# Kernel tuning notes

Hardware: AMD Instinct MI355X
Metric: run time of the kernel (lower is better)

## Reference

```python
import jax, jax.numpy as jnp
import numpy as np


def _relu(x):
    return jnp.maximum(x, 0.0)


def _wn(V, g):
    # torch weight_norm with dim=None: W = g * V / ||V||_F (scalar g)
    return g * V / jnp.linalg.norm(V)


def _wn_rank(V, g):
    # V: [rank, out, in], g: [rank] -> per-rank weight-normed weights
    n = jnp.sqrt(jnp.sum(V * V, axis=(1, 2), keepdims=True))
    return g[:, None, None] * V / n


def setup_inputs() -> dict:
    key = jax.random.key(0)
    ks = jax.random.split(key, 20)
    B, N, D, H, R, HK, G = 16, 64, 512, 512, 8, 64, 2
    f = lambda i, shape, s=1.0: jax.random.normal(ks[i], shape, dtype=jnp.float32) * s
    u = lambda i, shape: jax.random.uniform(ks[i], shape, dtype=jnp.float32)
    return {
        'v': f(0, (B, N, D)), 'q': f(1, (B, N, D)), 'a': f(2, (B, N, D)),
        'V_v': f(3, (H, D), 0.05), 'g_v': u(4, (1,)), 'b_v': f(5, (H,), 0.05),
        'V_q': f(6, (H, D), 0.05), 'g_q': u(7, (1,)), 'b_q': f(8, (H,), 0.05),
        'V_a': f(9, (H, D), 0.05), 'g_a': u(10, (1,)), 'b_a': f(11, (H,), 0.05),
        'Vn_v': f(12, (R, HK, H), 0.05), 'gn_v': u(13, (R,)), 'bn_v': f(14, (R, HK), 0.05),
        'Vn_qa': f(15, (R, HK, H), 0.05), 'gn_qa': u(16, (R,)), 'bn_qa': f(17, (R, HK), 0.05),
        'T_g': f(18, (R, HK, HK, HK, G), 0.02),  # T_g with h_out=1 squeezed
        'gamma': u(19, (H,)), 'beta': jnp.zeros((H,), jnp.float32),
    }


def reference(v, q, a, V_v, g_v, b_v, V_q, g_q, b_q, V_a, g_a, b_a,
              Vn_v, gn_v, bn_v, Vn_qa, gn_qa, bn_qa, T_g, gamma, beta):
    # Tucker projections (FCNet = weight-normed Linear + ReLU; dropout off in eval)
    v_t = _relu(v @ _wn(V_v, g_v).T + b_v)  # [B, Nv, H]
    q_t = _relu(q @ _wn(V_q, g_q).T + b_q)  # [B, Nq, H]
    a_t = _relu(a @ _wn(V_a, g_a).T + b_a)  # [B, Na, H]

    # Per-rank FCNets, vectorized over the rank loop (q_net and a_net share weights)
    Wv = _wn_rank(Vn_v, gn_v)    # [R, HK, H]
    Wqa = _wn_rank(Vn_qa, gn_qa)  # [R, HK, H]
    v_r = _relu(jnp.einsum('bnh,rkh->brnk', v_t, Wv) + bn_v[None, :, None, :])   # [B,R,Nv,HK]
    q_r = _relu(jnp.einsum('bnh,rkh->brnk', q_t, Wqa) + bn_qa[None, :, None, :])  # [B,R,Nq,HK]
    a_r = _relu(jnp.einsum('bnh,rkh->brnk', a_t, Wqa) + bn_qa[None, :, None, :])  # [B,R,Na,HK]

    # ModeProduct summed over rank: f_emb[b,v,q,m,g] = sum_r T_g[r,h,k,l,g] v_r q_r a_r
    t = jnp.einsum('brvh,rhklg->brvklg', v_r, T_g)
    t = jnp.einsum('brvklg,brqk->brvqlg', t, q_r)
    f_emb = jnp.einsum('brvqlg,brml->bvqmg', t, a_r)  # [B, Nv, Nq, Na, G]

    # logits = einsum('bdv,bvqag,bdqi,bdaj->bdijg').sum(-1).squeeze(3).squeeze(2)
    # with i=j=1 this is: logits[b,d] = sum_{v,q,a,g} v_t f_emb q_t a_t
    t2 = jnp.einsum('bvqag,bad->bvqdg', f_emb, a_t)
    t2 = jnp.einsum('bvqdg,bqd->bvdg', t2, q_t)
    logits = jnp.einsum('bvdg,bvd->bd', t2, v_t)  # [B, H]

    # BatchNorm1d (training-mode batch statistics, eps=1e-5)
    mu = jnp.mean(logits, axis=0)
    var = jnp.var(logits, axis=0)
    logits = (logits - mu) / jnp.sqrt(var + 1e-5) * gamma + beta

    # torch returns f_emb.squeeze(4): no-op since glimpse=2
    return f_emb, logits
```

## Files before the change

kernel.cpp:

```cpp
#include <hip/hip_runtime.h>
#include <hip/hip_fp16.h>
#include <math.h>


typedef _Float16 f16x8 __attribute__((ext_vector_type(8)));
typedef float f32x4 __attribute__((ext_vector_type(4)));

__device__ __forceinline__ unsigned short f2h(float x) {
  _Float16 h = (_Float16)x;
  return __builtin_bit_cast(unsigned short, h);
}

__device__ __forceinline__ int fragoff(int row, int kr) {
  return (((row & 15) + (((kr >> 2) & 3) << 4)) << 3) + (kr & 3) + (((kr >> 4) & 1) << 2);
}

#define WS_NRM 0
#define WS_VT  32
#define WS_QT  (WS_VT + 524288)
#define WS_AT  (WS_QT + 524288)
#define WS_LP  (WS_AT + 524288)
#define WS_LR  (WS_LP + 524288)
#define WS_PRT (WS_LR + 8192)
#define WS_H   (WS_PRT + 1280)
#define H_VR2 0
#define H_QR2 524288
#define H_AR2 1048576
#define H_T2  1572864
#define H_AT16 5767168
#define H_IN16 6291456
#define H_WB16 7864320
#define H_WN16 8650752
#define H_RP16 9175040
#define H_U   10747904

__global__ __launch_bounds__(256) void k_norms_part(
    const float* __restrict__ Vv, const float* __restrict__ Vq, const float* __restrict__ Va,
    const float* __restrict__ Vnv, const float* __restrict__ Vnqa, float* __restrict__ prt)
{
  const int bx = blockIdx.x;
  int n, j;
  const float* base;
  if (bx < 192) {
    n = bx >> 6; j = bx & 63;
    base = (n == 0 ? Vv : n == 1 ? Vq : Va) + j * 4096;
  } else {
    int t = bx - 192;
    n = 3 + (t >> 3); j = t & 7;
    base = (n < 11 ? Vnv + (n - 3) * 32768 : Vnqa + (n - 11) * 32768) + j * 4096;
  }
  const float4* p4 = (const float4*)base;
  float s = 0.f;
  #pragma unroll
  for (int i = 0; i < 4; ++i) {
    float4 x = p4[threadIdx.x + i * 256];
    s += x.x * x.x + x.y * x.y + x.z * x.z + x.w * x.w;
  }
  __shared__ float red[256];
  red[threadIdx.x] = s; __syncthreads();
  for (int off = 128; off > 0; off >>= 1) {
    if (threadIdx.x < off) red[threadIdx.x] += red[threadIdx.x + off];
    __syncthreads();
  }
  if (threadIdx.x == 0) prt[n * 64 + j] = red[0];
}

__global__ __launch_bounds__(64) void k_norms_fin(const float* __restrict__ prt, float* __restrict__ wsn)
{
  const int n = blockIdx.x, t = threadIdx.x;
  const int cnt = (n < 3) ? 64 : 8;
  float s = (t < cnt) ? prt[n * 64 + t] : 0.f;
  #pragma unroll
  for (int off = 32; off > 0; off >>= 1) s += __shfl_down(s, off);
  if (t == 0) wsn[n] = sqrtf(s);
}

__global__ __launch_bounds__(256) void k_inconv16(
    const float* __restrict__ v, const float* __restrict__ q, const float* __restrict__ a,
    unsigned short* __restrict__ IN16)
{
  const int z = blockIdx.y;
  const float4* src = (const float4*)((z == 0) ? v : (z == 1) ? q : a);
  #pragma unroll
  for (int i = 0; i < 8; ++i) {
    int f = blockIdx.x * 2048 + threadIdx.x + i * 256;
    int row = f >> 7, d0 = (f & 127) * 4;
    float4 x = src[f];
    ushort4 pk;
    pk.x = f2h(x.x); pk.y = f2h(x.y); pk.z = f2h(x.z); pk.w = f2h(x.w);
    int lanep = (row & 15) + (((d0 >> 2) & 3) << 4);
    int jb = ((d0 >> 4) & 1) << 2;
    size_t off = ((size_t)(z * 64 + (row >> 4)) * 16 + (d0 >> 5)) * 512 + lanep * 8 + jb;
    *(ushort4*)&IN16[off] = pk;
  }
}

__global__ __launch_bounds__(256) void k_wconv16(
    const float* __restrict__ Wv, const float* __restrict__ Wq, const float* __restrict__ Wa,
    const float* __restrict__ gv, const float* __restrict__ gq, const float* __restrict__ ga,
    const float* __restrict__ wsn, unsigned short* __restrict__ WB16)
{
  const int z = blockIdx.y;
  const float4* src = (const float4*)((z == 0) ? Wv : (z == 1) ? Wq : Wa);
  const float scale = ((z == 0) ? gv[0] : (z == 1) ? gq[0] : ga[0]) / wsn[z];
  #pragma unroll
  for (int i = 0; i < 8; ++i) {
    int f = blockIdx.x * 2048 + threadIdx.x + i * 256;
    int n = f >> 7, d0 = (f & 127) * 4;
    float4 x = src[f];
    ushort4 pk;
    pk.x = f2h(x.x * scale); pk.y = f2h(x.y * scale);
    pk.z = f2h(x.z * scale); pk.w = f2h(x.w * scale);
    int lanep = (n & 15) + (((d0 >> 2) & 3) << 4);
    int jb = ((d0 >> 4) & 1) << 2;
    size_t off = ((size_t)(z * 32 + (n >> 4)) * 16 + (d0 >> 5)) * 512 + lanep * 8 + jb;
    *(ushort4*)&WB16[off] = pk;
  }
}

__global__ __launch_bounds__(256) void k_wnconv16(
    const float* __restrict__ Vnv, const float* __restrict__ Vnqa,
    const float* __restrict__ gnv, const float* __restrict__ gnqa,
    const float* __restrict__ wsn, unsigned short* __restrict__ WN16)
{
  const int zr = blockIdx.x >> 2, sub = blockIdx.x & 3;
  const int zq = zr >> 3, r = zr & 7;
  const float4* src = (const float4*)((zq == 0 ? Vnv : Vnqa) + (size_t)r * 32768);
  const float scale = (zq == 0) ? (gnv[r] / wsn[3 + r]) : (gnqa[r] / wsn[11 + r]);
  #pragma unroll
  for (int i = 0; i < 8; ++i) {
    int f = sub * 2048 + threadIdx.x + i * 256;
    int n = f >> 7, d0 = (f & 127) * 4;
    float4 x = src[f];
    ushort4 pk;
    pk.x = f2h(x.x * scale); pk.y = f2h(x.y * scale);
    pk.z = f2h(x.z * scale); pk.w = f2h(x.w * scale);
    int lanep = (n & 15) + (((d0 >> 2) & 3) << 4);
    int jb = ((d0 >> 4) & 1) << 2;
    size_t off = ((size_t)(zr * 4 + (n >> 4)) * 16 + (d0 >> 5)) * 512 + lanep * 8 + jb;
    *(ushort4*)&WN16[off] = pk;
  }
}

__global__ __launch_bounds__(256) void k_repack2b(const float* __restrict__ Tg, unsigned short* __restrict__ T2)
{
  const int r = blockIdx.x >> 4, lB = blockIdx.x & 15;
  __shared__ unsigned short lds[32768];
  const int tid = threadIdx.x;

  #pragma unroll
  for (int i = 0; i < 32; ++i) {
    int f = tid + i * 256;
    int lpair = f & 1, k = (f >> 1) & 63, h = f >> 7;
    int l0 = lB * 4 + lpair * 2;
    const float4 x = *(const float4*)(Tg + ((size_t)((r * 64 + h) * 64 + k) * 64 + l0) * 2);
    const int el = fragoff(k & 15, h & 31);
    const int ks = h >> 5;
    const int ntr0 = (l0 & 3) * 4 + (k >> 4);
    const int ntr1 = ((l0 + 1) & 3) * 4 + (k >> 4);
    lds[((0 * 16 + ntr0) * 2 + ks) * 512 + el] = f2h(x.x);
    lds[((1 * 16 + ntr0) * 2 + ks) * 512 + el] = f2h(x.y);
    lds[((0 * 16 + ntr1) * 2 + ks) * 512 + el] = f2h(x.z);
    lds[((1 * 16 + ntr1) * 2 + ks) * 512 + el] = f2h(x.w);
  }
  __syncthreads();

  #pragma unroll
  for (int g = 0; g < 2; ++g) {
    unsigned short* dst = T2 + ((size_t)(g * 8 + r) * 256 + lB * 16) * 1024;
    const float4* s = (const float4*)&lds[g * 16384];
    float4* d = (float4*)dst;
    #pragma unroll
    for (int i = 0; i < 8; ++i) d[tid + i * 256] = s[tid + i * 256];
  }
}

__global__ __launch_bounds__(256) void k_proj16(
    const unsigned short* __restrict__ IN16, const unsigned short* __restrict__ WB16,
    const float* __restrict__ bv, const float* __restrict__ bq, const float* __restrict__ ba,
    float* __restrict__ ov, float* __restrict__ oq, float* __restrict__ oa,
    unsigned short* __restrict__ RP16, unsigned short* __restrict__ AT16)
{
  const int nB = blockIdx.x, mB = blockIdx.y, z = blockIdx.z;
  const float* bias = (z == 0) ? bv : (z == 1) ? bq : ba;
  float* out = (z == 0) ? ov : (z == 1) ? oq : oa;
  const int tid = threadIdx.x, lane = tid & 63;
  const int w = __builtin_amdgcn_readfirstlane(tid >> 6);

  f32x4 c[4];
  #pragma unroll
  for (int mt = 0; mt < 4; ++mt) c[mt] = (f32x4){0.f, 0.f, 0.f, 0.f};

  #pragma unroll 4
  for (int ks = 0; ks < 16; ++ks) {
    f16x8 af[4], bfr;
    #pragma unroll
    for (int mt = 0; mt < 4; ++mt)
      af[mt] = *(const f16x8*)&IN16[((size_t)(z * 64 + mB * 4 + mt) * 16 + ks) * 512 + lane * 8];
    bfr = *(const f16x8*)&WB16[((size_t)(z * 32 + nB * 4 + w) * 16 + ks) * 512 + lane * 8];
    #pragma unroll
    for (int mt = 0; mt < 4; ++mt)
      c[mt] = __builtin_amdgcn_mfma_f32_16x16x32_f16(af[mt], bfr, c[mt], 0, 0, 0);
  }

  const int col = nB * 64 + w * 16 + (lane & 15);
  const float bb = bias[col];
  #pragma unroll
  for (int mt = 0; mt < 4; ++mt)
    #pragma unroll
    for (int i = 0; i < 4; ++i) {
      const int row = mB * 64 + mt * 16 + 4 * (lane >> 4) + i;
      float val = fmaxf(c[mt][i] + bb, 0.f);
      unsigned short hv = f2h(val);
      out[(size_t)row * 512 + col] = val;
      RP16[((size_t)(z * 64 + (row >> 4)) * 16 + (col >> 5)) * 512 + fragoff(row, col & 31)] = hv;
      if (z == 2) {
        const int m = row & 63;
        AT16[(size_t)(row >> 6) * 32768 + ((col >> 4) * 2 + (m >> 5)) * 512 + fragoff(col & 15, m & 31)] = hv;
      }
    }
}

__global__ __launch_bounds__(256) void k_rproj16(
    const unsigned short* __restrict__ RP16, const unsigned short* __restrict__ WN16,
    const float* __restrict__ bnv, const float* __restrict__ bnqa,
    unsigned short* __restrict__ vrT2, unsigned short* __restrict__ qrT2,
    unsigned short* __restrict__ arT2)
{
  const int r = blockIdx.x, mB = blockIdx.y, z = blockIdx.z;
  const int zq = (z == 0) ? 0 : 1;
  const float* bias = ((z == 0) ? bnv : bnqa) + r * 64;
  const int tid = threadIdx.x, lane = tid & 63;
  const int w = __builtin_amdgcn_readfirstlane(tid >> 6);
  const int wm = w >> 1, wn = w & 1;

  f32x4 c[2][2];
  #pragma unroll
  for (int mi = 0; mi < 2; ++mi)
    #pragma unroll
    for (int ni = 0; ni < 2; ++ni) c[mi][ni] = (f32x4){0.f, 0.f, 0.f, 0.f};

  #pragma unroll 4
  for (int ks = 0; ks < 16; ++ks) {
    f16x8 af[2], bf[2];
    #pragma unroll
    for (int mi = 0; mi < 2; ++mi)
      af[mi] = *(const f16x8*)&RP16[((size_t)(z * 64 + mB * 4 + wm * 2 + mi) * 16 + ks) * 512 + lane * 8];
    #pragma unroll
    for (int ni = 0; ni < 2; ++ni)
      bf[ni] = *(const f16x8*)&WN16[((size_t)((zq * 8 + r) * 4 + wn * 2 + ni) * 16 + ks) * 512 + lane * 8];
    #pragma unroll
    for (int mi = 0; mi < 2; ++mi)
      #pragma unroll
      for (int ni = 0; ni < 2; ++ni)
        c[mi][ni] = __builtin_amdgcn_mfma_f32_16x16x32_f16(af[mi], bf[ni], c[mi][ni], 0, 0, 0);
  }

  #pragma unroll
  for (int mi = 0; mi < 2; ++mi)
    #pragma unroll
    for (int ni = 0; ni < 2; ++ni) {
      const int n = (wn * 2 + ni) * 16 + (lane & 15);
      const float bb2 = bias[n];
      #pragma unroll
      for (int i = 0; i < 4; ++i) {
        const int mm = mB * 64 + (wm * 2 + mi) * 16 + 4 * (lane >> 4) + i;
        const int bb = mm >> 6, nr = mm & 63;
        float val = fmaxf(c[mi][ni][i] + bb2, 0.f);
        unsigned short hv = f2h(val);
        if (z == 0)
          vrT2[(size_t)(bb * 8 + r) * 4096 + ((nr >> 4) * 2 + (n >> 5)) * 512 + fragoff(nr, n & 31)] = hv;
        else if (z == 1)
          qrT2[(size_t)(bb * 8 + r) * 4096 + ((nr >> 4) * 2 + (n >> 5)) * 512 + fragoff(nr, n & 31)] = hv;
        else
          arT2[(size_t)(((bb * 8 + r) * 2 + (n >> 5)) * 4 + (nr >> 4)) * 512 + fragoff(nr, n & 31)] = hv;
      }
    }
}

__global__ __launch_bounds__(512) void k_stage1(
    const unsigned short* __restrict__ vrT2, const unsigned short* __restrict__ T2,
    unsigned short* __restrict__ U)
{
  const int b = blockIdx.x, rq = blockIdx.y, z = blockIdx.z;
  const int ntB = z & 3, g = (z >> 2) & 1, rh = z >> 3;
  const int r = rh * 4 + rq;
  const int tid = threadIdx.x, lane = tid & 63;
  const int w = __builtin_amdgcn_readfirstlane(tid >> 6);

  __shared__ __align__(16) unsigned short VR[4096];
  __shared__ __align__(16) unsigned short TC[16384];
  __shared__ __align__(16) unsigned short ST[16384];

  {
    const float4* s = (const float4*)(vrT2 + (size_t)(b * 8 + r) * 4096);
    *(float4*)&VR[tid * 8] = s[tid];
  }

  const size_t t2base = ((size_t)(g * 8 + r) * 256 + ntB * 64) * 1024;

  for (int sb = 0; sb < 4; ++sb) {
    {
      const float4* s = (const float4*)(T2 + t2base + (size_t)sb * 16384);
      float4* d = (float4*)TC;
      #pragma unroll
      for (int i = 0; i < 4; ++i) d[tid + i * 512] = s[tid + i * 512];
    }
    __syncthreads();

    f32x4 c[4][2];
    #pragma unroll
    for (int mt = 0; mt < 4; ++mt)
      #pragma unroll
      for (int nt = 0; nt < 2; ++nt)
        c[mt][nt] = (f32x4){0.f, 0.f, 0.f, 0.f};

    f16x8 af[4][2], bf[2][2];
    #pragma unroll
    for (int mt = 0; mt < 4; ++mt)
      #pragma unroll
      for (int ks = 0; ks < 2; ++ks)
        af[mt][ks] = *(const f16x8*)&VR[mt * 1024 + ks * 512 + lane * 8];
    #pragma unroll
    for (int nt = 0; nt < 2; ++nt)
      #pragma unroll
      for (int ks = 0; ks < 2; ++ks)
        bf[nt][ks] = *(const f16x8*)&TC[(w * 2 + nt) * 1024 + ks * 512 + lane * 8];

    #pragma unroll
    for (int mt = 0; mt < 4; ++mt)
      #pragma unroll
      for (int nt = 0; nt < 2; ++nt)
        #pragma unroll
        for (int ks = 0; ks < 2; ++ks)
          c[mt][nt] = __builtin_amdgcn_mfma_f32_16x16x32_f16(af[mt][ks], bf[nt][ks], c[mt][nt], 0, 0, 0);

    #pragma unroll
    for (int mt = 0; mt < 4; ++mt)
      #pragma unroll
      for (int nt = 0; nt < 2; ++nt) {
        const int Nt = ntB * 64 + sb * 16 + w * 2 + nt;
        const int n = Nt * 16 + (lane & 15);
        const int l = n >> 6, k = n & 63;
        #pragma unroll
        for (int i = 0; i < 4; ++i) {
          const int v = mt * 16 + 4 * (lane >> 4) + i;
          const int row16 = 8 * (l & 1) + (v & 7);
          const int el = ((v >> 3) * 2 + ((l >> 1) & 1)) * 1024 + (k >> 5) * 512 + fragoff(row16, k & 31);
          ST[el] = f2h(c[mt][nt][i]);
        }
      }
    __syncthreads();

    {
      const int l0 = ntB * 16 + sb * 4;
      const int lc = l0 >> 5;
      const int mtU0 = (l0 >> 1) & 15;
      const int rg = tid >> 5, idx = tid & 31;
      const int vt = rg >> 1, mtrel = rg & 1;
      unsigned short* dst = U + ((size_t)((((g * 16 + b) * 8 + vt) * 8 + r) * 2 + lc)) * 16384
                              + (size_t)(mtU0 + mtrel) * 1024;
      const float4* s = (const float4*)&ST[rg * 1024];
      float4* d = (float4*)dst;
      #pragma unroll
      for (int i = 0; i < 4; ++i) d[idx + i * 32] = s[idx + i * 32];
    }
    __syncthreads();
  }
}

__global__ __launch_bounds__(512) void k_stage23(
    const unsigned short* __restrict__ U, const unsigned short* __restrict__ qrT2,
    const unsigned short* __restrict__ arT2, float* __restrict__ fout)
{
  const int b = blockIdx.x, vt = blockIdx.y, g = blockIdx.z;
  const int tid = threadIdx.x, lane = tid & 63;
  const int w = __builtin_amdgcn_readfirstlane(tid >> 6);

  __shared__ __align__(16) unsigned short UA[16384];
  __shared__ __align__(16) unsigned short QB[4096];
  __shared__ __align__(16) unsigned short AB[2048];
  __shared__ __align__(16) unsigned short CC[8192];

  f32x4 f[2][2][4];
  #pragma unroll
  for (int qh = 0; qh < 2; ++qh)
    #pragma unroll
    for (int qt = 0; qt < 2; ++qt)
      #pragma unroll
      for (int nt = 0; nt < 4; ++nt)
        f[qh][qt][nt] = (f32x4){0.f, 0.f, 0.f, 0.f};

  for (int r = 0; r < 8; ++r) {
    const float4* sq = (const float4*)(qrT2 + (size_t)(b * 8 + r) * 4096);

    for (int lc = 0; lc < 2; ++lc) {
      {
        const float4* su = (const float4*)(U + ((size_t)((((g * 16 + b) * 8 + vt) * 8 + r) * 2 + lc)) * 16384);
        float4* du = (float4*)UA;
        #pragma unroll
        for (int i = 0; i < 4; ++i) du[tid + i * 512] = su[tid + i * 512];
      }
      {
        const float4* sa = (const float4*)(arT2 + ((size_t)((b * 8 + r) * 2 + lc)) * 2048);
        if (tid < 256) ((float4*)AB)[tid] = sa[tid];
      }
      if (lc == 0 && tid >= 256) {
        ((float4*)QB)[tid - 256] = sq[tid - 256];
        ((float4*)QB)[tid] = sq[tid];
      }
      __syncthreads();

      f16x8 b3[4];
      #pragma unroll
      for (int nt = 0; nt < 4; ++nt)
        b3[nt] = *(const f16x8*)&AB[nt * 512 + lane * 8];

      f16x8 a2[2][2];
      #pragma unroll
      for (int mi = 0; mi < 2; ++mi)
        #pragma unroll
        for (int ks = 0; ks < 2; ++ks)
          a2[mi][ks] = *(const f16x8*)&UA[(w * 2 + mi) * 1024 + ks * 512 + lane * 8];

      #pragma unroll
      for (int qh = 0; qh < 2; ++qh) {
        f32x4 c2[2][2];
        #pragma unroll
        for (int mi = 0; mi < 2; ++mi)
          #pragma unroll
          for (int nt = 0; nt < 2; ++nt)
            c2[mi][nt] = (f32x4){0.f, 0.f, 0.f, 0.f};

        f16x8 b2[2][2];
        #pragma unroll
        for (int nt = 0; nt < 2; ++nt)
          #pragma unroll
          for (int ks = 0; ks < 2; ++ks)
            b2[nt][ks] = *(const f16x8*)&QB[(qh * 2 + nt) * 1024 + ks * 512 + lane * 8];

        #pragma unroll
        for (int mi = 0; mi < 2; ++mi)
          #pragma unroll
          for (int nt = 0; nt < 2; ++nt)
            #pragma unroll
            for (int ks = 0; ks < 2; ++ks)
              c2[mi][nt] = __builtin_amdgcn_mfma_f32_16x16x32_f16(a2[mi][ks], b2[nt][ks], c2[mi][nt], 0, 0, 0);

        #pragma unroll
        for (int mi = 0; mi < 2; ++mi)
          #pragma unroll
          for (int nt = 0; nt < 2; ++nt)
            #pragma unroll
            for (int i = 0; i < 4; ++i) {
              const int row = (w * 2 + mi) * 16 + 4 * (lane >> 4) + i;
              const int l = row >> 3, v = row & 7;
              const int el = (v * 2 + nt) * 512 + fragoff(lane & 15, l);
              CC[el] = f2h(c2[mi][nt][i]);
            }
        __syncthreads();

        f16x8 a3[2];
        #pragma unroll
        for (int qt = 0; qt < 2; ++qt)
          a3[qt] = *(const f16x8*)&CC[(w * 2 + qt) * 512 + lane * 8];

        #pragma unroll
        for (int qt = 0; qt < 2; ++qt)
          #pragma unroll
          for (int nt = 0; nt < 4; ++nt)
            f[qh][qt][nt] = __builtin_amdgcn_mfma_f32_16x16x32_f16(a3[qt], b3[nt], f[qh][qt][nt], 0, 0, 0);
        __syncthreads();
      }
    }
  }

  #pragma unroll
  for (int qh = 0; qh < 2; ++qh)
    #pragma unroll
    for (int qt = 0; qt < 2; ++qt)
      #pragma unroll
      for (int nt = 0; nt < 4; ++nt)
        #pragma unroll
        for (int i = 0; i < 4; ++i) {
          const int q = qh * 32 + qt * 16 + 4 * (lane >> 4) + i;
          const int m = nt * 16 + (lane & 15);
          size_t addr = ((((size_t)b * 64 + vt * 8 + w) * 64 + q) * 64 + m) * 2 + g;
          fout[addr] = f[qh][qt][nt][i];
        }
}

__global__ __launch_bounds__(512) void k_logits2(
    const float* __restrict__ vt, const float* __restrict__ qt,
    const unsigned short* __restrict__ AT16, const float* __restrict__ fout,
    float* __restrict__ Lp)
{
  const int v = blockIdx.x, b = blockIdx.y;
  const int tid = threadIdx.x, lane = tid & 63;
  const int w = __builtin_amdgcn_readfirstlane(tid >> 6);

  __shared__ __align__(16) unsigned int FAu[2048];

  {
    const float4* fo4 = (const float4*)(fout + ((size_t)(b * 64 + v)) * 8192);
    #pragma unroll
    for (int i = 0; i < 4; ++i) {
      int fi = tid + i * 512;
      int q = fi >> 5, mpair = fi & 31;
      float4 x = fo4[fi];
      float s0 = x.x + x.y, s1 = x.z + x.w;
      int m0 = mpair * 2;
      int off = fragoff(q & 15, m0 & 31);
      int idx2 = (((q >> 4) * 2 + (m0 >> 5)) * 512 + off) >> 1;
      unsigned int pk = (unsigned int)f2h(s0) | ((unsigned int)f2h(s1) << 16);
      FAu[idx2] = pk;
    }
  }
  __syncthreads();

  const unsigned short* FAh = (const unsigned short*)FAu;

  f16x8 af[4][2], bf[4][2];
  #pragma unroll
  for (int mt = 0; mt < 4; ++mt)
    #pragma unroll
    for (int ks = 0; ks < 2; ++ks)
      af[mt][ks] = *(const f16x8*)&FAh[(mt * 2 + ks) * 512 + lane * 8];
  #pragma unroll
  for (int nt = 0; nt < 4; ++nt)
    #pragma unroll
    for (int ks = 0; ks < 2; ++ks)
      bf[nt][ks] = *(const f16x8*)&AT16[(size_t)((b * 32 + w * 4 + nt) * 2 + ks) * 512 + lane * 8];

  f32x4 c[4][4];
  #pragma unroll
  for (int mt = 0; mt < 4; ++mt)
    #pragma unroll
    for (int nt = 0; nt < 4; ++nt)
      c[mt][nt] = (f32x4){0.f, 0.f, 0.f, 0.f};

  #pragma unroll
  for (int mt = 0; mt < 4; ++mt)
    #pragma unroll
    for (int nt = 0; nt < 4; ++nt)
      #pragma unroll
      for (int ks = 0; ks < 2; ++ks)
        c[mt][nt] = __builtin_amdgcn_mfma_f32_16x16x32_f16(af[mt][ks], bf[nt][ks], c[mt][nt], 0, 0, 0);

  const int gr = lane >> 4, dl = lane & 15;
  #pragma unroll
  for (int nt = 0; nt < 4; ++nt) {
    const int d = w * 64 + nt * 16 + dl;
    float partial = 0.f;
    #pragma unroll
    for (int mt = 0; mt < 4; ++mt) {
      #pragma unroll
      for (int i = 0; i < 4; ++i) {
        const int q = mt * 16 + gr * 4 + i;
        partial += qt[(b * 64 + q) * 512 + d] * c[mt][nt][i];
      }
    }
    partial += __shfl_xor(partial, 16);
    partial += __shfl_xor(partial, 32);
    const float val = vt[(b * 64 + v) * 512 + d] * partial;
    if (lane < 16) Lp[((size_t)(b * 64 + v)) * 512 + d] = val;
  }
}

__global__ __launch_bounds__(512) void k_lred(const float* __restrict__ Lp, float* __restrict__ Lraw)
{
  const int b = blockIdx.x, d = threadIdx.x;
  float s = 0.f;
  for (int v = 0; v < 64; ++v) s += Lp[(size_t)(b * 64 + v) * 512 + d];
  Lraw[b * 512 + d] = s;
}

__global__ __launch_bounds__(512) void k_bn(
    const float* __restrict__ Lraw, const float* __restrict__ gamma,
    const float* __restrict__ beta, float* __restrict__ lout)
{
  const int d = threadIdx.x;
  float x[16]; float mu = 0.f;
  #pragma unroll
  for (int b = 0; b < 16; ++b) { x[b] = Lraw[b * 512 + d]; mu += x[b]; }
  mu *= (1.f / 16.f);
  float var = 0.f;
  #pragma unroll
  for (int b = 0; b < 16; ++b) { float t = x[b] - mu; var += t * t; }
  var *= (1.f / 16.f);
  const float sc = gamma[d] / sqrtf(var + 1e-5f);
  const float bt = beta[d];
  #pragma unroll
  for (int b = 0; b < 16; ++b) lout[b * 512 + d] = (x[b] - mu) * sc + bt;
}

extern "C" void kernel_launch(void* const* d_in, const int* in_sizes, int n_in,
                              void* d_out, int out_size, void* d_ws, size_t ws_size,
                              hipStream_t stream)
{
  const float* v    = (const float*)d_in[0];
  const float* q    = (const float*)d_in[1];
  const float* a    = (const float*)d_in[2];
  const float* Vv   = (const float*)d_in[3];
  const float* gv   = (const float*)d_in[4];
  const float* bv   = (const float*)d_in[5];
  const float* Vq   = (const float*)d_in[6];
  const float* gq   = (const float*)d_in[7];
  const float* bq   = (const float*)d_in[8];
  const float* Va   = (const float*)d_in[9];
  const float* ga   = (const float*)d_in[10];
  const float* ba   = (const float*)d_in[11];
  const float* Vnv  = (const float*)d_in[12];
  const float* gnv  = (const float*)d_in[13];
  const float* bnv  = (const float*)d_in[14];
  const float* Vnqa = (const float*)d_in[15];
  const float* gnqa = (const float*)d_in[16];
  const float* bnqa = (const float*)d_in[17];
  const float* Tg   = (const float*)d_in[18];
  const float* gamma= (const float*)d_in[19];
  const float* beta = (const float*)d_in[20];

  float* ws   = (float*)d_ws;
  unsigned short* hb = (unsigned short*)(ws + WS_H);
  float* fout = (float*)d_out;
  float* lout = fout + (size_t)16 * 64 * 64 * 64 * 2;

  k_norms_part<<<320, 256, 0, stream>>>(Vv, Vq, Va, Vnv, Vnqa, ws + WS_PRT);
  k_norms_fin<<<19, 64, 0, stream>>>(ws + WS_PRT, ws + WS_NRM);
  k_inconv16<<<dim3(64, 3), 256, 0, stream>>>(v, q, a, hb + H_IN16);
  k_wconv16<<<dim3(32, 3), 256, 0, stream>>>(Vv, Vq, Va, gv, gq, ga, ws + WS_NRM, hb + H_WB16);
  k_wnconv16<<<64, 256, 0, stream>>>(Vnv, Vnqa, gnv, gnqa, ws + WS_NRM, hb + H_WN16);
  k_repack2b<<<128, 256, 0, stream>>>(Tg, hb + H_T2);
  k_proj16<<<dim3(8, 16, 3), 256, 0, stream>>>(hb + H_IN16, hb + H_WB16, bv, bq, ba,
                                               ws + WS_VT, ws + WS_QT, ws + WS_AT,
                                               hb + H_RP16, hb + H_AT16);
  k_rproj16<<<dim3(8, 16, 3), 256, 0, stream>>>(hb + H_RP16, hb + H_WN16, bnv, bnqa,
                                                hb + H_VR2, hb + H_QR2, hb + H_AR2);
  k_stage1<<<dim3(16, 4, 16), 512, 0, stream>>>(hb + H_VR2, hb + H_T2, hb + H_U);
  k_stage23<<<dim3(16, 8, 2), 512, 0, stream>>>(hb + H_U, hb + H_QR2, hb + H_AR2, fout);
  k_logits2<<<dim3(64, 16), 512, 0, stream>>>(ws + WS_VT, ws + WS_QT,
                                              hb + H_AT16, fout, ws + WS_LP);
  k_lred<<<16, 512, 0, stream>>>(ws + WS_LP, ws + WS_LR);
  k_bn<<<1, 512, 0, stream>>>(ws + WS_LR, gamma, beta, lout);
}
```

Measured before the change: 161.5 us.

## Fuse Tucker stage1 into stage23 to compute U on the fly in LDS

Drops the separate stage1 kernel, which wrote the large intermediate U tensor to global memory. The combined kernel now computes each 8-row slice of v_r times T_g with MFMA directly into LDS, then runs the q and a contractions as before. v_r is stored in a plain row-major layout and gathered into MFMA fragments per rank. This removes the U global round trip and one launch, but each block re-reads its T_g slices from global memory, and only 8 of 16 MFMA rows are useful, which wastes matrix throughput.

```diff
diff --git a/kernel.cpp b/kernel.cpp
--- a/kernel.cpp
+++ b/kernel.cpp
@@ -23,7 +23,7 @@
 #define WS_LR  (WS_LP + 524288)
 #define WS_PRT (WS_LR + 8192)
 #define WS_H   (WS_PRT + 1280)
-#define H_VR2 0
+#define H_VRL 0
 #define H_QR2 524288
 #define H_AR2 1048576
 #define H_T2  1572864
@@ -32,7 +32,6 @@
 #define H_WB16 7864320
 #define H_WN16 8650752
 #define H_RP16 9175040
-#define H_U   10747904
 
 __global__ __launch_bounds__(256) void k_norms_part(
     const float* __restrict__ Vv, const float* __restrict__ Vq, const float* __restrict__ Va,
@@ -224,7 +223,7 @@
 __global__ __launch_bounds__(256) void k_rproj16(
     const unsigned short* __restrict__ RP16, const unsigned short* __restrict__ WN16,
     const float* __restrict__ bnv, const float* __restrict__ bnqa,
-    unsigned short* __restrict__ vrT2, unsigned short* __restrict__ qrT2,
+    unsigned short* __restrict__ vrLin, unsigned short* __restrict__ qrT2,
     unsigned short* __restrict__ arT2)
 {
   const int r = blockIdx.x, mB = blockIdx.y, z = blockIdx.z;
@@ -269,7 +268,7 @@
         float val = fmaxf(c[mi][ni][i] + bb2, 0.f);
         unsigned short hv = f2h(val);
         if (z == 0)
-          vrT2[(size_t)(bb * 8 + r) * 4096 + ((nr >> 4) * 2 + (n >> 5)) * 512 + fragoff(nr, n & 31)] = hv;
+          vrLin[((size_t)(bb * 8 + r) * 64 + nr) * 64 + n] = hv;
         else if (z == 1)
           qrT2[(size_t)(bb * 8 + r) * 4096 + ((nr >> 4) * 2 + (n >> 5)) * 512 + fragoff(nr, n & 31)] = hv;
         else
@@ -278,100 +277,10 @@
     }
 }
 
-__global__ __launch_bounds__(512) void k_stage1(
-    const unsigned short* __restrict__ vrT2, const unsigned short* __restrict__ T2,
-    unsigned short* __restrict__ U)
-{
-  const int b = blockIdx.x, rq = blockIdx.y, z = blockIdx.z;
-  const int ntB = z & 3, g = (z >> 2) & 1, rh = z >> 3;
-  const int r = rh * 4 + rq;
-  const int tid = threadIdx.x, lane = tid & 63;
-  const int w = __builtin_amdgcn_readfirstlane(tid >> 6);
-
-  __shared__ __align__(16) unsigned short VR[4096];
-  __shared__ __align__(16) unsigned short TC[16384];
-  __shared__ __align__(16) unsigned short ST[16384];
-
-  {
-    const float4* s = (const float4*)(vrT2 + (size_t)(b * 8 + r) * 4096);
-    *(float4*)&VR[tid * 8] = s[tid];
-  }
-
-  const size_t t2base = ((size_t)(g * 8 + r) * 256 + ntB * 64) * 1024;
-
-  for (int sb = 0; sb < 4; ++sb) {
-    {
-      const float4* s = (const float4*)(T2 + t2base + (size_t)sb * 16384);
-      float4* d = (float4*)TC;
-      #pragma unroll
-      for (int i = 0; i < 4; ++i) d[tid + i * 512] = s[tid + i * 512];
-    }
-    __syncthreads();
-
-    f32x4 c[4][2];
-    #pragma unroll
-    for (int mt = 0; mt < 4; ++mt)
-      #pragma unroll
-      for (int nt = 0; nt < 2; ++nt)
-        c[mt][nt] = (f32x4){0.f, 0.f, 0.f, 0.f};
-
-    f16x8 af[4][2], bf[2][2];
-    #pragma unroll
-    for (int mt = 0; mt < 4; ++mt)
-      #pragma unroll
-      for (int ks = 0; ks < 2; ++ks)
-        af[mt][ks] = *(const f16x8*)&VR[mt * 1024 + ks * 512 + lane * 8];
-    #pragma unroll
-    for (int nt = 0; nt < 2; ++nt)
-      #pragma unroll
-      for (int ks = 0; ks < 2; ++ks)
-        bf[nt][ks] = *(const f16x8*)&TC[(w * 2 + nt) * 1024 + ks * 512 + lane * 8];
-
-    #pragma unroll
-    for (int mt = 0; mt < 4; ++mt)
-      #pragma unroll
-      for (int nt = 0; nt < 2; ++nt)
-        #pragma unroll
-        for (int ks = 0; ks < 2; ++ks)
-          c[mt][nt] = __builtin_amdgcn_mfma_f32_16x16x32_f16(af[mt][ks], bf[nt][ks], c[mt][nt], 0, 0, 0);
-
-    #pragma unroll
-    for (int mt = 0; mt < 4; ++mt)
-      #pragma unroll
-      for (int nt = 0; nt < 2; ++nt) {
-        const int Nt = ntB * 64 + sb * 16 + w * 2 + nt;
-        const int n = Nt * 16 + (lane & 15);
-        const int l = n >> 6, k = n & 63;
-        #pragma unroll
-        for (int i = 0; i < 4; ++i) {
-          const int v = mt * 16 + 4 * (lane >> 4) + i;
-          const int row16 = 8 * (l & 1) + (v & 7);
-          const int el = ((v >> 3) * 2 + ((l >> 1) & 1)) * 1024 + (k >> 5) * 512 + fragoff(row16, k & 31);
-          ST[el] = f2h(c[mt][nt][i]);
-        }
-      }
-    __syncthreads();
-
-    {
-      const int l0 = ntB * 16 + sb * 4;
-      const int lc = l0 >> 5;
-      const int mtU0 = (l0 >> 1) & 15;
-      const int rg = tid >> 5, idx = tid & 31;
-      const int vt = rg >> 1, mtrel = rg & 1;
-      unsigned short* dst = U + ((size_t)((((g * 16 + b) * 8 + vt) * 8 + r) * 2 + lc)) * 16384
-                              + (size_t)(mtU0 + mtrel) * 1024;
-      const float4* s = (const float4*)&ST[rg * 1024];
-      float4* d = (float4*)dst;
-      #pragma unroll
-      for (int i = 0; i < 4; ++i) d[idx + i * 32] = s[idx + i * 32];
-    }
-    __syncthreads();
-  }
-}
-
-__global__ __launch_bounds__(512) void k_stage23(
-    const unsigned short* __restrict__ U, const unsigned short* __restrict__ qrT2,
-    const unsigned short* __restrict__ arT2, float* __restrict__ fout)
+__global__ __launch_bounds__(512) void k_tucker16(
+    const unsigned short* __restrict__ vrLin, const unsigned short* __restrict__ qrT2,
+    const unsigned short* __restrict__ arT2, const unsigned short* __restrict__ T2,
+    float* __restrict__ fout)
 {
   const int b = blockIdx.x, vt = blockIdx.y, g = blockIdx.z;
   const int tid = threadIdx.x, lane = tid & 63;
@@ -381,6 +290,7 @@
   __shared__ __align__(16) unsigned short QB[4096];
   __shared__ __align__(16) unsigned short AB[2048];
   __shared__ __align__(16) unsigned short CC[8192];
+  __shared__ __align__(16) unsigned short VRL[512];
 
   f32x4 f[2][2][4];
   #pragma unroll
@@ -392,31 +302,62 @@
         f[qh][qt][nt] = (f32x4){0.f, 0.f, 0.f, 0.f};
 
   for (int r = 0; r < 8; ++r) {
-    const float4* sq = (const float4*)(qrT2 + (size_t)(b * 8 + r) * 4096);
+    if (tid < 64)
+      *(float4*)&VRL[tid * 8] =
+          ((const float4*)(vrLin + (size_t)(b * 8 + r) * 4096 + vt * 512))[tid];
+    *(float4*)&QB[tid * 8] = ((const float4*)(qrT2 + (size_t)(b * 8 + r) * 4096))[tid];
+    __syncthreads();
+
+    f16x8 af1[2];
+    #pragma unroll
+    for (int ks = 0; ks < 2; ++ks)
+      #pragma unroll
+      for (int j = 0; j < 8; ++j) {
+        const int kr = (j & 3) + ((lane >> 4) & 3) * 4 + (j >> 2) * 16;
+        af1[ks][j] = __builtin_bit_cast(_Float16, VRL[(lane & 7) * 64 + ks * 32 + kr]);
+      }
 
     for (int lc = 0; lc < 2; ++lc) {
-      {
-        const float4* su = (const float4*)(U + ((size_t)((((g * 16 + b) * 8 + vt) * 8 + r) * 2 + lc)) * 16384);
-        float4* du = (float4*)UA;
-        #pragma unroll
-        for (int i = 0; i < 4; ++i) du[tid + i * 512] = su[tid + i * 512];
-      }
-      {
-        const float4* sa = (const float4*)(arT2 + ((size_t)((b * 8 + r) * 2 + lc)) * 2048);
-        if (tid < 256) ((float4*)AB)[tid] = sa[tid];
-      }
-      if (lc == 0 && tid >= 256) {
-        ((float4*)QB)[tid - 256] = sq[tid - 256];
-        ((float4*)QB)[tid] = sq[tid];
+      if (tid < 256)
+        ((float4*)AB)[tid] = ((const float4*)(arT2 + ((size_t)((b * 8 + r) * 2 + lc)) * 2048))[tid];
+
+      const unsigned short* tb = T2 + ((size_t)((g * 8 + r) * 256 + lc * 128 + w * 16)) * 1024;
+      for (int tg = 0; tg < 4; ++tg) {
+        f16x8 bf[4][2];
+        f32x4 d[4];
+        #pragma unroll
+        for (int tt = 0; tt < 4; ++tt) {
+          #pragma unroll
+          for (int ks = 0; ks < 2; ++ks)
+            bf[tt][ks] = *(const f16x8*)&tb[(size_t)(tg * 4 + tt) * 1024 + ks * 512 + lane * 8];
+          d[tt] = (f32x4){0.f, 0.f, 0.f, 0.f};
+        }
+        #pragma unroll
+        for (int tt = 0; tt < 4; ++tt)
+          #pragma unroll
+          for (int ks = 0; ks < 2; ++ks)
+            d[tt] = __builtin_amdgcn_mfma_f32_16x16x32_f16(af1[ks], bf[tt][ks], d[tt], 0, 0, 0);
+        if (lane < 32) {
+          #pragma unroll
+          for (int tt = 0; tt < 4; ++tt) {
+            const int t = w * 16 + tg * 4 + tt;
+            const int lrel = t >> 2;
+            const int k0 = (t & 3) * 16 + (lane & 15);
+            #pragma unroll
+            for (int i = 0; i < 4; ++i) {
+              const int v = 4 * (lane >> 4) + i;
+              const int row = lrel * 8 + v;
+              UA[(row >> 4) * 1024 + (k0 >> 5) * 512 + fragoff(row & 15, k0 & 31)] = f2h(d[tt][i]);
+            }
+          }
+        }
       }
       __syncthreads();
 
-      f16x8 b3[4];
+      f16x8 b3[4], a2[2][2];
       #pragma unroll
       for (int nt = 0; nt < 4; ++nt)
         b3[nt] = *(const f16x8*)&AB[nt * 512 + lane * 8];
-
-      f16x8 a2[2][2];
       #pragma unroll
       for (int mi = 0; mi < 2; ++mi)
         #pragma unroll
@@ -635,9 +576,9 @@
                                                ws + WS_VT, ws + WS_QT, ws + WS_AT,
                                                hb + H_RP16, hb + H_AT16);
   k_rproj16<<<dim3(8, 16, 3), 256, 0, stream>>>(hb + H_RP16, hb + H_WN16, bnv, bnqa,
-                                                hb + H_VR2, hb + H_QR2, hb + H_AR2);
-  k_stage1<<<dim3(16, 4, 16), 512, 0, stream>>>(hb + H_VR2, hb + H_T2, hb + H_U);
-  k_stage23<<<dim3(16, 8, 2), 512, 0, stream>>>(hb + H_U, hb + H_QR2, hb + H_AR2, fout);
+                                                hb + H_VRL, hb + H_QR2, hb + H_AR2);
+  k_tucker16<<<dim3(16, 8, 2), 512, 0, stream>>>(hb + H_VRL, hb + H_QR2, hb + H_AR2,
+                                                 hb + H_T2, fout);
   k_logits2<<<dim3(64, 16), 512, 0, stream>>>(ws + WS_VT, ws + WS_QT,
                                               hb + H_AT16, fout, ws + WS_LP);
   k_lred<<<16, 512, 0, stream>>>(ws + WS_LP, ws + WS_LR);
```

After: 156.7 us. 3.0% less time.
